# Optimization experiments

Measured on AMD Instinct MI355X. Metric: run time of the kernel, lower is better.

Reference implementation:

```python
import jax, jax.numpy as jnp
import numpy as np

EPS_BN = 1e-5  # torch BatchNorm1d default eps
EPS_W = 1e-8   # dist reciprocal eps from source


def _bn_relu(x, gamma, beta):
    # x: [B, C, N]; training-mode batchnorm (biased var over B and N per channel)
    mean = jnp.mean(x, axis=(0, 2), keepdims=True)
    var = jnp.mean((x - mean) ** 2, axis=(0, 2), keepdims=True)
    xn = (x - mean) * jax.lax.rsqrt(var + EPS_BN)
    return jax.nn.relu(xn * gamma[None, :, None] + beta[None, :, None])


def setup_inputs() -> dict:
    key = jax.random.key(0)
    ks = jax.random.split(key, 12)
    B, N, S, D = 2, 16384, 4096, 256
    mlp = [256, 256]
    in_ch = 2 * D
    inp = {
        'xyz1': jax.random.normal(ks[0], (B, 3, N), jnp.float32),
        'xyz2': jax.random.normal(ks[1], (B, 3, S), jnp.float32),
        'points1': jax.random.normal(ks[2], (B, D, N), jnp.float32),
        'points2': jax.random.normal(ks[3], (B, D, S), jnp.float32),
    }
    last = in_ch
    for i, out in enumerate(mlp):
        inp[f'W{i}'] = jax.random.normal(ks[4 + 2 * i], (out, last), jnp.float32) * (1.0 / np.sqrt(last))
        inp[f'b{i}'] = jnp.zeros((out,), jnp.float32)
        inp[f'g{i}'] = jnp.ones((out,), jnp.float32)
        inp[f'be{i}'] = jnp.zeros((out,), jnp.float32)
        last = out
    return inp


def reference(xyz1, xyz2, points1, points2, W0, b0, g0, be0, W1, b1, g1, be1):
    B = xyz1.shape[0]
    p1 = jnp.swapaxes(xyz1, 1, 2)      # [B, N, 3]
    p2 = jnp.swapaxes(xyz2, 1, 2)      # [B, S, 3]
    f2 = jnp.swapaxes(points2, 1, 2)   # [B, S, D]

    # square_distance: ||a||^2 + ||b||^2 - 2 a.b  -> [B, N, S]
    d = (jnp.sum(p1 * p1, -1)[:, :, None]
         + jnp.sum(p2 * p2, -1)[:, None, :]
         - 2.0 * jnp.einsum('bnc,bsc->bns', p1, p2))

    # 3 nearest neighbors (same math as full sort + [:, :, :3])
    neg_top, idx = jax.lax.top_k(-d, 3)       # [B, N, 3]
    dists = -neg_top
    w = 1.0 / (dists + EPS_W)
    w = w / jnp.sum(w, axis=2, keepdims=True)  # [B, N, 3]

    # gather neighbor features: [B, N, 3, D]
    gathered = f2[jnp.arange(B)[:, None, None], idx]
    interp = jnp.sum(gathered * w[..., None], axis=2)   # [B, N, D]

    # concat skip features along channels -> [B, D1+D2, N]
    new_points = jnp.concatenate([points1, jnp.swapaxes(interp, 1, 2)], axis=1)

    # 1x1 conv + BN(train) + ReLU stack
    for W, b, g, be in ((W0, b0, g0, be0), (W1, b1, g1, be1)):
        new_points = _bn_relu(jnp.einsum('oc,bcn->bon', W, new_points) + b[None, :, None], g, be)
    return new_points
```

## Files before the change

kernel.cpp:

```cpp
#include <hip/hip_runtime.h>

#define NCHUNK 16

typedef __attribute__((ext_vector_type(8))) short bf16x8;
typedef __attribute__((ext_vector_type(4))) float f32x4;
typedef __attribute__((ext_vector_type(2))) float f32x2;
typedef __attribute__((ext_vector_type(8))) short short8v;

struct PairRec { f32x2 x, y, z, w; };

__device__ __forceinline__ unsigned short f2bf(float f){
  union { float f; unsigned u; } v; v.f = f;
  unsigned u = v.u;
  u += 0x7FFFu + ((u >> 16) & 1u);
  return (unsigned short)(u >> 16);
}

__device__ __forceinline__ float bf2f(unsigned short h){
  union { unsigned u; float f; } v; v.u = ((unsigned)h) << 16;
  return v.f;
}

__device__ __forceinline__ void gl_lds16(const void* g, void* l){
  __builtin_amdgcn_global_load_lds((const __attribute__((address_space(1))) unsigned*)g,
                                   (__attribute__((address_space(3))) unsigned*)l, 16, 0, 0);
}

__device__ __forceinline__ f32x2 pkdist(PairRec p, f32x2 qx2, f32x2 qy2, f32x2 qz2, f32x2 r12){
  f32x2 dot = p.x * qx2;
  dot = __builtin_elementwise_fma(p.y, qy2, dot);
  dot = __builtin_elementwise_fma(p.z, qz2, dot);
  f32x2 t = r12 + p.w;
  f32x2 n2 = {-2.0f, -2.0f};
  return __builtin_elementwise_fma(dot, n2, t);
}

__device__ __forceinline__ void ins3(float d, int s,
    float& m0, float& m1, float& m2, int& i0, int& i1, int& i2){
  bool c0 = d < m0, c1 = d < m1, c2 = d < m2;
  float om0 = m0, om1 = m1;
  m0 = fminf(om0, d);
  m1 = __builtin_amdgcn_fmed3f(om0, om1, d);
  m2 = __builtin_amdgcn_fmed3f(om1, m2, d);
  int j1 = c0 ? i0 : s;
  int j2 = c1 ? i1 : s;
  i0 = c0 ? s  : i0;
  i1 = c1 ? j1 : i1;
  i2 = c2 ? j2 : i2;
}

__global__ __launch_bounds__(256) void k_convert_w(const float* __restrict__ W0, const float* __restrict__ W1,
                            unsigned short* __restrict__ W0b, unsigned short* __restrict__ W1b,
                            const float* __restrict__ xyz2, float* __restrict__ p2pp){
  int i = blockIdx.x*256 + threadIdx.x;
  if (i < 256*512) W0b[i] = f2bf(W0[i]);
  if (i < 256*256) W1b[i] = f2bf(W1[i]);
  if (i < 8192){
    int b = i >> 12, s = i & 4095;
    const float* px = xyz2 + (size_t)b*3*4096;
    float x = px[s], y = px[4096+s], z = px[8192+s];
    float r2 = x*x + y*y + z*z;
    size_t base = (size_t)b*16384 + (size_t)(s >> 1)*8 + (s & 1);
    p2pp[base+0] = x; p2pp[base+2] = y; p2pp[base+4] = z; p2pp[base+6] = r2;
  }
}

__global__ __launch_bounds__(256) void k_tp2(const float* __restrict__ p2, float* __restrict__ f2t){
  __shared__ float tile[64][65];
  int bx = blockIdx.x;
  int by = blockIdx.y;
  int b  = blockIdx.z;
  int t = threadIdx.x; int tx = t & 63; int ty = t >> 6;
  const float* src = p2 + ((size_t)b*256 + by*64)*4096 + bx*64;
  #pragma unroll
  for (int i = 0; i < 16; ++i){
    int c = ty*16 + i;
    tile[c][tx] = src[(size_t)c*4096 + tx];
  }
  __syncthreads();
  float* dst = f2t + ((size_t)b*4096 + (size_t)bx*64)*256 + by*64;
  #pragma unroll
  for (int i = 0; i < 16; ++i){
    int s = ty*16 + i;
    dst[(size_t)s*256 + tx] = tile[tx][s];
  }
}

__global__ __launch_bounds__(256) void k_tp1(const float* __restrict__ p1, unsigned short* __restrict__ Xt){
  __shared__ float tile[64][65];
  int bx = blockIdx.x;
  int by = blockIdx.y;
  int b  = blockIdx.z;
  int t = threadIdx.x; int tx = t & 63; int ty = t >> 6;
  const float* src = p1 + ((size_t)b*256 + by*64)*16384 + (size_t)bx*64;
  #pragma unroll
  for (int i = 0; i < 16; ++i){
    int c = ty*16 + i;
    tile[c][tx] = src[(size_t)c*16384 + tx];
  }
  __syncthreads();
  unsigned short* dst = Xt + ((size_t)b*16384 + (size_t)bx*64)*512 + by*64;
  #pragma unroll
  for (int i = 0; i < 16; ++i){
    int n = ty*16 + i;
    dst[(size_t)n*512 + tx] = f2bf(tile[tx][n]);
  }
}

__global__ __launch_bounds__(256) void k_knn(const float* __restrict__ xyz1, const float* __restrict__ p2pp,
                      float* __restrict__ pd, int* __restrict__ pi){
  int b = blockIdx.z, cc = blockIdx.y;
  int n = blockIdx.x*256 + threadIdx.x;
  const float* q = xyz1 + (size_t)b*3*16384;
  float qx = q[n], qy = q[16384+n], qz = q[32768+n];
  float r1 = qx*qx + qy*qy + qz*qz;
  f32x2 qx2 = {qx,qx}, qy2 = {qy,qy}, qz2 = {qz,qz}, r12 = {r1,r1};
  const int NP = (4096/NCHUNK)/2;
  int s0 = cc*(4096/NCHUNK);
  const PairRec* pp = (const PairRec*)p2pp + (size_t)b*2048 + cc*NP;
  float m0=3.4e38f, m1=3.4e38f, m2=3.4e38f;
  int i0=0, i1=0, i2=0;
  for (int g = 0; g < NP/4; ++g){
    PairRec pA = pp[g*4+0], pB = pp[g*4+1], pC = pp[g*4+2], pD = pp[g*4+3];
    int sb = s0 + g*8;
    f32x2 dA = pkdist(pA, qx2, qy2, qz2, r12);
    ins3(dA.x, sb+0, m0,m1,m2, i0,i1,i2);
    ins3(dA.y, sb+1, m0,m1,m2, i0,i1,i2);
    f32x2 dB = pkdist(pB, qx2, qy2, qz2, r12);
    ins3(dB.x, sb+2, m0,m1,m2, i0,i1,i2);
    ins3(dB.y, sb+3, m0,m1,m2, i0,i1,i2);
    f32x2 dC = pkdist(pC, qx2, qy2, qz2, r12);
    ins3(dC.x, sb+4, m0,m1,m2, i0,i1,i2);
    ins3(dC.y, sb+5, m0,m1,m2, i0,i1,i2);
    f32x2 dD = pkdist(pD, qx2, qy2, qz2, r12);
    ins3(dD.x, sb+6, m0,m1,m2, i0,i1,i2);
    ins3(dD.y, sb+7, m0,m1,m2, i0,i1,i2);
  }
  size_t base = (((size_t)b*16384 + n)*NCHUNK + cc)*3;
  pd[base]=m0; pd[base+1]=m1; pd[base+2]=m2;
  pi[base]=i0; pi[base+1]=i1; pi[base+2]=i2;
}

__global__ __launch_bounds__(256) void k_knn_merge(const float* __restrict__ pd, const int* __restrict__ pi,
                            int* __restrict__ ki, float* __restrict__ kw){
  size_t qq = (size_t)blockIdx.x*256 + threadIdx.x;
  float d0=3.4e38f,d1=3.4e38f,d2=3.4e38f; int i0=0,i1=0,i2=0;
  size_t base = qq*NCHUNK*3;
  for (int c = 0; c < NCHUNK*3; ++c){
    float d = pd[base+c]; int s = pi[base+c];
    if (d < d2){
      if (d < d1){
        d2=d1; i2=i1;
        if (d < d0){ d1=d0; i1=i0; d0=d; i0=s; }
        else       { d1=d; i1=s; }
      } else { d2=d; i2=s; }
    }
  }
  float w0 = 1.0f/(d0+1e-8f), w1 = 1.0f/(d1+1e-8f), w2 = 1.0f/(d2+1e-8f);
  float inv = 1.0f/(w0+w1+w2);
  size_t kb = qq*3;
  ki[kb]=i0; ki[kb+1]=i1; ki[kb+2]=i2;
  kw[kb]=w0*inv; kw[kb+1]=w1*inv; kw[kb+2]=w2*inv;
}

__global__ __launch_bounds__(256) void k_interp(const float* __restrict__ f2t, const int* __restrict__ ki,
                         const float* __restrict__ kw, unsigned short* __restrict__ Xt){
  int t = threadIdx.x;
  int g = t >> 6; int lane = t & 63;
  size_t q = (size_t)blockIdx.x*4 + g;
  int b = (int)(q >> 14);
  const float* f2 = f2t + (size_t)b*4096*256;
  size_t kb = q*3;
  int i0 = ki[kb], i1 = ki[kb+1], i2 = ki[kb+2];
  float w0 = kw[kb], w1 = kw[kb+1], w2 = kw[kb+2];
  const float4 a = *(const float4*)(f2 + (size_t)i0*256 + lane*4);
  const float4 c = *(const float4*)(f2 + (size_t)i1*256 + lane*4);
  const float4 e = *(const float4*)(f2 + (size_t)i2*256 + lane*4);
  ushort4 o;
  o.x = f2bf(w0*a.x + w1*c.x + w2*e.x);
  o.y = f2bf(w0*a.y + w1*c.y + w2*e.y);
  o.z = f2bf(w0*a.z + w1*c.z + w2*e.z);
  o.w = f2bf(w0*a.w + w1*c.w + w2*e.w);
  *(ushort4*)(Xt + q*512 + 256 + lane*4) = o;
}

template<int K>
__global__ __launch_bounds__(256) void k_gemm(const unsigned short* __restrict__ A,
                       const unsigned short* __restrict__ Bm,
                       unsigned short* __restrict__ Cb,
                       float* __restrict__ psum, float* __restrict__ psq){
  __shared__ unsigned short As[128*32];
  __shared__ unsigned short Bs[128*32];
  __shared__ float redS[2][128];
  __shared__ float redQ[2][128];
  int t = threadIdx.x;
  int bo = blockIdx.x * 128;
  size_t bn = (size_t)blockIdx.y * 128;
  int w = t >> 6, l = t & 63;
  int wr = w >> 1, wc = w & 1;
  f32x4 acc[4][4] = {};

  const char* Ap = (const char*)A;
  const char* Bp = (const char*)Bm;
  int r0 = t >> 2;
  int cb = (t & 3) * 16;
  for (int k0 = 0; k0 < K; k0 += 32){
    __syncthreads();
    #pragma unroll
    for (int p = 0; p < 2; ++p){
      int off = (t + p*256)*16;
      int r = r0 + p*64;
      gl_lds16(Ap + (size_t)(bo + r)*(K*2) + (size_t)k0*2 + cb, (char*)As + off);
      gl_lds16(Bp + (bn + r)*(K*2) + (size_t)k0*2 + cb, (char*)Bs + off);
    }
    __syncthreads();
    bf16x8 af[4], bfr[4];
    int lr = l & 15, lk = (l >> 4) * 8;
    #pragma unroll
    for (int mt = 0; mt < 4; ++mt)
      af[mt] = *(const bf16x8*)(As + (wr*64 + mt*16 + lr)*32 + lk);
    #pragma unroll
    for (int nt = 0; nt < 4; ++nt)
      bfr[nt] = *(const bf16x8*)(Bs + (wc*64 + nt*16 + lr)*32 + lk);
    #pragma unroll
    for (int mt = 0; mt < 4; ++mt)
      #pragma unroll
      for (int nt = 0; nt < 4; ++nt)
        acc[mt][nt] = __builtin_amdgcn_mfma_f32_16x16x32_bf16(af[mt], bfr[nt], acc[mt][nt], 0, 0, 0);
  }
  int lo = (l >> 4) * 4, ln = l & 15;
  #pragma unroll
  for (int mt = 0; mt < 4; ++mt){
    #pragma unroll
    for (int nt = 0; nt < 4; ++nt){
      size_t n = bn + wc*64 + nt*16 + ln;
      int o = bo + wr*64 + mt*16 + lo;
      ushort4 ov;
      ov.x = f2bf(acc[mt][nt][0]); ov.y = f2bf(acc[mt][nt][1]);
      ov.z = f2bf(acc[mt][nt][2]); ov.w = f2bf(acc[mt][nt][3]);
      *(ushort4*)(Cb + n*256 + o) = ov;
    }
  }
  float ps[16], pq[16];
  #pragma unroll
  for (int mt = 0; mt < 4; ++mt){
    #pragma unroll
    for (int j = 0; j < 4; ++j){
      float s = 0.f, qv = 0.f;
      #pragma unroll
      for (int nt = 0; nt < 4; ++nt){
        float v = acc[mt][nt][j];
        s += v; qv += v*v;
      }
      ps[mt*4+j] = s; pq[mt*4+j] = qv;
    }
  }
  #pragma unroll
  for (int dlt = 1; dlt < 16; dlt <<= 1){
    #pragma unroll
    for (int i = 0; i < 16; ++i){
      ps[i] += __shfl_xor(ps[i], dlt);
      pq[i] += __shfl_xor(pq[i], dlt);
    }
  }
  if ((l & 15) == 0){
    #pragma unroll
    for (int mt = 0; mt < 4; ++mt){
      #pragma unroll
      for (int j = 0; j < 4; ++j){
        int ol = wr*64 + mt*16 + (l>>4)*4 + j;
        redS[wc][ol] = ps[mt*4+j];
        redQ[wc][ol] = pq[mt*4+j];
      }
    }
  }
  __syncthreads();
  if (t < 128){
    psum[(size_t)(bo + t)*256 + blockIdx.y] = redS[0][t] + redS[1][t];
    psq [(size_t)(bo + t)*256 + blockIdx.y] = redQ[0][t] + redQ[1][t];
  }
}

__global__ __launch_bounds__(256) void k_gemm2(const unsigned short* __restrict__ A,
                       const unsigned short* __restrict__ C1,
                       const float* __restrict__ scale, const float* __restrict__ shift,
                       unsigned short* __restrict__ Cb,
                       float* __restrict__ psum, float* __restrict__ psq){
  const int K = 256;
  __shared__ unsigned short As[128*32];
  __shared__ unsigned short Bs[128*32];
  __shared__ float redS[2][128];
  __shared__ float redQ[2][128];
  int t = threadIdx.x;
  int bo = blockIdx.x * 128;
  size_t bn = (size_t)blockIdx.y * 128;
  int w = t >> 6, l = t & 63;
  int wr = w >> 1, wc = w & 1;
  f32x4 acc[4][4] = {};

  const char* Ap = (const char*)A;
  int r0 = t >> 2;
  int cb = (t & 3) * 16;
  int ce0 = (t & 3) * 8;
  for (int k0 = 0; k0 < K; k0 += 32){
    int ce = k0 + ce0;
    float4 a0 = *(const float4*)(scale+ce); float4 a1 = *(const float4*)(scale+ce+4);
    float4 b0 = *(const float4*)(shift+ce); float4 b1 = *(const float4*)(shift+ce+4);
    float sc[8] = {a0.x,a0.y,a0.z,a0.w,a1.x,a1.y,a1.z,a1.w};
    float sh[8] = {b0.x,b0.y,b0.z,b0.w,b1.x,b1.y,b1.z,b1.w};
    short8v vin[2];
    #pragma unroll
    for (int p = 0; p < 2; ++p){
      int r = r0 + p*64;
      vin[p] = *(const short8v*)(C1 + (bn + r)*256 + ce);
    }
    __syncthreads();
    #pragma unroll
    for (int p = 0; p < 2; ++p){
      int r = r0 + p*64;
      gl_lds16(Ap + (size_t)(bo + r)*(K*2) + (size_t)k0*2 + cb, (char*)As + (t + p*256)*16);
    }
    #pragma unroll
    for (int p = 0; p < 2; ++p){
      short8v pv;
      #pragma unroll
      for (int j = 0; j < 8; ++j){
        float y = fmaxf(0.f, bf2f((unsigned short)vin[p][j])*sc[j] + sh[j]);
        pv[j] = (short)f2bf(y);
      }
      *(short8v*)((char*)Bs + (t + p*256)*16) = pv;
    }
    __syncthreads();
    bf16x8 af[4], bfr[4];
    int lr = l & 15, lk = (l >> 4) * 8;
    #pragma unroll
    for (int mt = 0; mt < 4; ++mt)
      af[mt] = *(const bf16x8*)(As + (wr*64 + mt*16 + lr)*32 + lk);
    #pragma unroll
    for (int nt = 0; nt < 4; ++nt)
      bfr[nt] = *(const bf16x8*)(Bs + (wc*64 + nt*16 + lr)*32 + lk);
    #pragma unroll
    for (int mt = 0; mt < 4; ++mt)
      #pragma unroll
      for (int nt = 0; nt < 4; ++nt)
        acc[mt][nt] = __builtin_amdgcn_mfma_f32_16x16x32_bf16(af[mt], bfr[nt], acc[mt][nt], 0, 0, 0);
  }
  int lo = (l >> 4) * 4, ln = l & 15;
  #pragma unroll
  for (int mt = 0; mt < 4; ++mt){
    #pragma unroll
    for (int nt = 0; nt < 4; ++nt){
      size_t n = bn + wc*64 + nt*16 + ln;
      int o = bo + wr*64 + mt*16 + lo;
      ushort4 ov;
      ov.x = f2bf(acc[mt][nt][0]); ov.y = f2bf(acc[mt][nt][1]);
      ov.z = f2bf(acc[mt][nt][2]); ov.w = f2bf(acc[mt][nt][3]);
      *(ushort4*)(Cb + n*256 + o) = ov;
    }
  }
  float ps[16], pq[16];
  #pragma unroll
  for (int mt = 0; mt < 4; ++mt){
    #pragma unroll
    for (int j = 0; j < 4; ++j){
      float s = 0.f, qv = 0.f;
      #pragma unroll
      for (int nt = 0; nt < 4; ++nt){
        float v = acc[mt][nt][j];
        s += v; qv += v*v;
      }
      ps[mt*4+j] = s; pq[mt*4+j] = qv;
    }
  }
  #pragma unroll
  for (int dlt = 1; dlt < 16; dlt <<= 1){
    #pragma unroll
    for (int i = 0; i < 16; ++i){
      ps[i] += __shfl_xor(ps[i], dlt);
      pq[i] += __shfl_xor(pq[i], dlt);
    }
  }
  if ((l & 15) == 0){
    #pragma unroll
    for (int mt = 0; mt < 4; ++mt){
      #pragma unroll
      for (int j = 0; j < 4; ++j){
        int ol = wr*64 + mt*16 + (l>>4)*4 + j;
        redS[wc][ol] = ps[mt*4+j];
        redQ[wc][ol] = pq[mt*4+j];
      }
    }
  }
  __syncthreads();
  if (t < 128){
    psum[(size_t)(bo + t)*256 + blockIdx.y] = redS[0][t] + redS[1][t];
    psq [(size_t)(bo + t)*256 + blockIdx.y] = redQ[0][t] + redQ[1][t];
  }
}

__global__ __launch_bounds__(256) void k_stats_f(const float* __restrict__ psum, const float* __restrict__ psq,
                          const float* __restrict__ gamma, const float* __restrict__ beta,
                          float* __restrict__ scale, float* __restrict__ shift){
  int o = blockIdx.x; int t = threadIdx.x;
  float s = psum[(size_t)o*256 + t];
  float q = psq [(size_t)o*256 + t];
  #pragma unroll
  for (int d = 1; d < 64; d <<= 1){
    s += __shfl_xor(s, d);
    q += __shfl_xor(q, d);
  }
  __shared__ float ls[4], lq[4];
  if ((t & 63) == 0){ ls[t>>6] = s; lq[t>>6] = q; }
  __syncthreads();
  if (t == 0){
    float S = ls[0]+ls[1]+ls[2]+ls[3];
    float Q = lq[0]+lq[1]+lq[2]+lq[3];
    const float invc = 1.0f/32768.0f;
    float mean = S*invc;
    float var = Q*invc - mean*mean;
    float sc = gamma[o]*rsqrtf(var + 1e-5f);
    scale[o] = sc;
    shift[o] = beta[o] - mean*sc;
  }
}

__global__ __launch_bounds__(256) void k_bn_out(const unsigned short* __restrict__ Cb, const float* __restrict__ scale,
                         const float* __restrict__ shift, float* __restrict__ out){
  __shared__ float tile[64][65];
  int bx = blockIdx.x;
  int by = blockIdx.y;
  int b  = blockIdx.z;
  int t = threadIdx.x; int tx = t & 63; int ty = t >> 6;
  const unsigned short* src = Cb + ((size_t)b*16384 + (size_t)bx*64)*256 + by*64;
  int o = by*64 + tx;
  float sc = scale[o], sh = shift[o];
  #pragma unroll
  for (int i = 0; i < 16; ++i){
    int n = ty*16 + i;
    float v = bf2f(src[(size_t)n*256 + tx]);
    tile[n][tx] = fmaxf(0.f, v*sc + sh);
  }
  __syncthreads();
  float* dst = out + ((size_t)b*256 + by*64)*16384 + (size_t)bx*64;
  #pragma unroll
  for (int i = 0; i < 16; ++i){
    int oo = ty*16 + i;
    dst[(size_t)oo*16384 + tx] = tile[tx][oo];
  }
}

extern "C" void kernel_launch(void* const* d_in, const int* in_sizes, int n_in,
                              void* d_out, int out_size, void* d_ws, size_t ws_size,
                              hipStream_t stream){
  const float* xyz1    = (const float*)d_in[0];
  const float* xyz2    = (const float*)d_in[1];
  const float* points1 = (const float*)d_in[2];
  const float* points2 = (const float*)d_in[3];
  const float* W0  = (const float*)d_in[4];
  const float* g0  = (const float*)d_in[6];
  const float* be0 = (const float*)d_in[7];
  const float* W1  = (const float*)d_in[8];
  const float* g1  = (const float*)d_in[10];
  const float* be1 = (const float*)d_in[11];

  char* w = (char*)d_ws;
  size_t o = 0;
  float* f2t = (float*)(w + o); o += 8388608;
  float* p2pp= (float*)(w + o); o += 131072;
  int*   kidx= (int*)(w + o);   o += 393216;
  float* kww = (float*)(w + o); o += 393216;
  unsigned short* W0b = (unsigned short*)(w + o); o += 262144;
  unsigned short* W1b = (unsigned short*)(w + o); o += 131072;
  float* psum = (float*)(w + o); o += 262144;
  float* psq  = (float*)(w + o); o += 262144;
  float* scale1 = (float*)(w + o); o += 1024;
  float* shift1 = (float*)(w + o); o += 1024;
  float* scale2 = (float*)(w + o); o += 1024;
  float* shift2 = (float*)(w + o); o += 1024;
  float* kpd = (float*)(w + o); o += 6291456;
  int*   kpi = (int*)(w + o);   o += 6291456;
  unsigned short* Xt = (unsigned short*)(w + o); size_t xto = o; o += 33554432;
  unsigned short* C1b = (unsigned short*)(w + o); o += 16777216;
  unsigned short* C2b = (unsigned short*)(w + xto);

  k_convert_w<<<512, 256, 0, stream>>>(W0, W1, W0b, W1b, xyz2, p2pp);
  k_tp2<<<dim3(64,4,2), 256, 0, stream>>>(points2, f2t);
  k_knn<<<dim3(64,NCHUNK,2), 256, 0, stream>>>(xyz1, p2pp, kpd, kpi);
  k_knn_merge<<<128, 256, 0, stream>>>(kpd, kpi, kidx, kww);
  k_tp1<<<dim3(256,4,2), 256, 0, stream>>>(points1, Xt);
  k_interp<<<8192, 256, 0, stream>>>(f2t, kidx, kww, Xt);
  k_gemm<512><<<dim3(2,256), 256, 0, stream>>>(W0b, Xt, C1b, psum, psq);
  k_stats_f<<<256, 256, 0, stream>>>(psum, psq, g0, be0, scale1, shift1);
  k_gemm2<<<dim3(2,256), 256, 0, stream>>>(W1b, C1b, scale1, shift1, C2b, psum, psq);
  k_stats_f<<<256, 256, 0, stream>>>(psum, psq, g1, be1, scale2, shift2);
  k_bn_out<<<dim3(256,4,2), 256, 0, stream>>>(C2b, scale2, shift2, (float*)d_out);
}
```

Before: 159.8 us.

## Fuse points1 transpose and bf16 conversion into first GEMM's B-tile load

Removes the separate k_tp1 kernel that transposed points1 into a bf16 staging buffer. The first GEMM now reads fp32 points1 directly for the first 256 K-channels, converts to bf16 and writes the transposed B tile into LDS itself. Interpolated features go to their own buffer and are loaded with global-to-LDS copies for the remaining channels. This saves one launch and a 16 MB write/read round trip, but each GEMM block (two per column tile) now repeats the fp32 load and conversion, and the LDS stores are scattered 4-byte writes that may cause bank conflicts.

```diff
diff --git a/kernel.cpp b/kernel.cpp
--- a/kernel.cpp
+++ b/kernel.cpp
@@ -83,27 +83,6 @@
   for (int i = 0; i < 16; ++i){
     int s = ty*16 + i;
     dst[(size_t)s*256 + tx] = tile[tx][s];
-  }
-}
-
-__global__ __launch_bounds__(256) void k_tp1(const float* __restrict__ p1, unsigned short* __restrict__ Xt){
-  __shared__ float tile[64][65];
-  int bx = blockIdx.x;
-  int by = blockIdx.y;
-  int b  = blockIdx.z;
-  int t = threadIdx.x; int tx = t & 63; int ty = t >> 6;
-  const float* src = p1 + ((size_t)b*256 + by*64)*16384 + (size_t)bx*64;
-  #pragma unroll
-  for (int i = 0; i < 16; ++i){
-    int c = ty*16 + i;
-    tile[c][tx] = src[(size_t)c*16384 + tx];
-  }
-  __syncthreads();
-  unsigned short* dst = Xt + ((size_t)b*16384 + (size_t)bx*64)*512 + by*64;
-  #pragma unroll
-  for (int i = 0; i < 16; ++i){
-    int n = ty*16 + i;
-    dst[(size_t)n*512 + tx] = f2bf(tile[tx][n]);
   }
 }
 
@@ -164,7 +143,7 @@
 }
 
 __global__ __launch_bounds__(256) void k_interp(const float* __restrict__ f2t, const int* __restrict__ ki,
-                         const float* __restrict__ kw, unsigned short* __restrict__ Xt){
+                         const float* __restrict__ kw, unsigned short* __restrict__ Yi){
   int t = threadIdx.x;
   int g = t >> 6; int lane = t & 63;
   size_t q = (size_t)blockIdx.x*4 + g;
@@ -181,14 +160,15 @@
   o.y = f2bf(w0*a.y + w1*c.y + w2*e.y);
   o.z = f2bf(w0*a.z + w1*c.z + w2*e.z);
   o.w = f2bf(w0*a.w + w1*c.w + w2*e.w);
-  *(ushort4*)(Xt + q*512 + 256 + lane*4) = o;
-}
-
-template<int K>
-__global__ __launch_bounds__(256) void k_gemm(const unsigned short* __restrict__ A,
-                       const unsigned short* __restrict__ Bm,
+  *(ushort4*)(Yi + q*256 + lane*4) = o;
+}
+
+__global__ __launch_bounds__(256) void k_gemm1(const unsigned short* __restrict__ A,
+                       const float* __restrict__ p1,
+                       const unsigned short* __restrict__ Yi,
                        unsigned short* __restrict__ Cb,
                        float* __restrict__ psum, float* __restrict__ psq){
+  const int K = 512;
   __shared__ unsigned short As[128*32];
   __shared__ unsigned short Bs[128*32];
   __shared__ float redS[2][128];
@@ -196,22 +176,46 @@
   int t = threadIdx.x;
   int bo = blockIdx.x * 128;
   size_t bn = (size_t)blockIdx.y * 128;
+  int b = (int)(bn >> 14);
+  int nn0 = (int)(bn & 16383);
   int w = t >> 6, l = t & 63;
   int wr = w >> 1, wc = w & 1;
   f32x4 acc[4][4] = {};
 
   const char* Ap = (const char*)A;
-  const char* Bp = (const char*)Bm;
   int r0 = t >> 2;
-  int cb = (t & 3) * 16;
+  int cbb = (t & 3) * 16;
+  int pch = t & 15;
+  int seg = t >> 4;
   for (int k0 = 0; k0 < K; k0 += 32){
     __syncthreads();
     #pragma unroll
     for (int p = 0; p < 2; ++p){
       int off = (t + p*256)*16;
       int r = r0 + p*64;
-      gl_lds16(Ap + (size_t)(bo + r)*(K*2) + (size_t)k0*2 + cb, (char*)As + off);
-      gl_lds16(Bp + (bn + r)*(K*2) + (size_t)k0*2 + cb, (char*)Bs + off);
+      gl_lds16(Ap + (size_t)(bo + r)*(K*2) + (size_t)k0*2 + cbb, (char*)As + off);
+    }
+    if (k0 < 256){
+      const float* s0 = p1 + ((size_t)(b*256 + k0 + 2*pch))*16384 + nn0 + seg*8;
+      const float* s1 = s0 + 16384;
+      float4 a0 = *(const float4*)(s0);
+      float4 a1 = *(const float4*)(s0+4);
+      float4 c0 = *(const float4*)(s1);
+      float4 c1 = *(const float4*)(s1+4);
+      float e0[8] = {a0.x,a0.y,a0.z,a0.w,a1.x,a1.y,a1.z,a1.w};
+      float e1[8] = {c0.x,c0.y,c0.z,c0.w,c1.x,c1.y,c1.z,c1.w};
+      #pragma unroll
+      for (int i = 0; i < 8; ++i){
+        unsigned v = ((unsigned)f2bf(e1[i]) << 16) | (unsigned)f2bf(e0[i]);
+        *(unsigned*)((char*)Bs + (size_t)(seg*8 + i)*64 + pch*4) = v;
+      }
+    } else {
+      #pragma unroll
+      for (int p = 0; p < 2; ++p){
+        int off = (t + p*256)*16;
+        int r = r0 + p*64;
+        gl_lds16((const char*)Yi + (bn + r)*512 + (size_t)(k0-256)*2 + cbb, (char*)Bs + off);
+      }
     }
     __syncthreads();
     bf16x8 af[4], bfr[4];
@@ -300,7 +304,7 @@
 
   const char* Ap = (const char*)A;
   int r0 = t >> 2;
-  int cb = (t & 3) * 16;
+  int cbb = (t & 3) * 16;
   int ce0 = (t & 3) * 8;
   for (int k0 = 0; k0 < K; k0 += 32){
     int ce = k0 + ce0;
@@ -318,7 +322,7 @@
     #pragma unroll
     for (int p = 0; p < 2; ++p){
       int r = r0 + p*64;
-      gl_lds16(Ap + (size_t)(bo + r)*(K*2) + (size_t)k0*2 + cb, (char*)As + (t + p*256)*16);
+      gl_lds16(Ap + (size_t)(bo + r)*(K*2) + (size_t)k0*2 + cbb, (char*)As + (t + p*256)*16);
     }
     #pragma unroll
     for (int p = 0; p < 2; ++p){
@@ -479,17 +483,16 @@
   float* shift2 = (float*)(w + o); o += 1024;
   float* kpd = (float*)(w + o); o += 6291456;
   int*   kpi = (int*)(w + o);   o += 6291456;
-  unsigned short* Xt = (unsigned short*)(w + o); size_t xto = o; o += 33554432;
+  unsigned short* Yi  = (unsigned short*)(w + o); o += 16777216;
   unsigned short* C1b = (unsigned short*)(w + o); o += 16777216;
-  unsigned short* C2b = (unsigned short*)(w + xto);
+  unsigned short* C2b = (unsigned short*)(w + o); o += 16777216;
 
   k_convert_w<<<512, 256, 0, stream>>>(W0, W1, W0b, W1b, xyz2, p2pp);
   k_tp2<<<dim3(64,4,2), 256, 0, stream>>>(points2, f2t);
   k_knn<<<dim3(64,NCHUNK,2), 256, 0, stream>>>(xyz1, p2pp, kpd, kpi);
   k_knn_merge<<<128, 256, 0, stream>>>(kpd, kpi, kidx, kww);
-  k_tp1<<<dim3(256,4,2), 256, 0, stream>>>(points1, Xt);
-  k_interp<<<8192, 256, 0, stream>>>(f2t, kidx, kww, Xt);
-  k_gemm<512><<<dim3(2,256), 256, 0, stream>>>(W0b, Xt, C1b, psum, psq);
+  k_interp<<<8192, 256, 0, stream>>>(f2t, kidx, kww, Yi);
+  k_gemm1<<<dim3(2,256), 256, 0, stream>>>(W0b, points1, Yi, C1b, psum, psq);
   k_stats_f<<<256, 256, 0, stream>>>(psum, psq, g0, be0, scale1, shift1);
   k_gemm2<<<dim3(2,256), 256, 0, stream>>>(W1b, C1b, scale1, shift1, C2b, psum, psq);
   k_stats_f<<<256, 256, 0, stream>>>(psum, psq, g1, be1, scale2, shift2);
```

Measured after the change: 156.1 us. 1.02x faster.
